# Performance work log

Measured on AMD Instinct MI355X. Metric: run time of the kernel, lower is better.

## Reference

```python
import jax, jax.numpy as jnp
import numpy as np

B, T, D, H = 4, 2048, 512, 8
K = D // H  # head dim = 64

def setup_inputs() -> dict:
    key = jax.random.key(0)
    k1, k2, k3, k4 = jax.random.split(key, 4)
    x = jax.random.normal(k1, (B, T, D), dtype=jnp.float32)
    # torch nn.Linear stores weight as [out_features, in_features]
    w_qkv = jax.random.normal(k2, (3 * D, D), dtype=jnp.float32) * (D ** -0.5)
    w_proj = jax.random.normal(k3, (D, D), dtype=jnp.float32) * (D ** -0.5)
    b_proj = jax.random.normal(k4, (D,), dtype=jnp.float32) * 0.01
    return {"x": x, "w_qkv": w_qkv, "w_proj": w_proj, "b_proj": b_proj}

def reference(x, w_qkv, w_proj, b_proj):
    Bx, Tx, Dx = x.shape
    # qkv projection (no bias): [B,T,3D]
    qkv = jnp.einsum('btd,ed->bte', x, w_qkv)
    q, k, v = jnp.split(qkv, 3, axis=-1)
    # [B,H,T,K]
    def heads(t):
        return t.reshape(Bx, Tx, H, K).transpose(0, 2, 1, 3)
    q, k, v = heads(q), heads(k), heads(v)
    # scaled scores with causal mask
    scores = jnp.einsum('bhqk,bhsk->bhqs', q, k) * (K ** -0.5)  # [B,H,T,T]
    causal = jnp.tril(jnp.ones((Tx, Tx), dtype=bool))
    scores = jnp.where(causal, scores, -jnp.inf)
    attn = jax.nn.softmax(scores, axis=-1)  # dropout p=0.0 -> identity
    out = jnp.einsum('bhqs,bhsk->bhqk', attn, v)  # [B,H,T,K]
    out = out.transpose(0, 2, 1, 3).reshape(Bx, Tx, Dx)
    out = jnp.einsum('btd,ed->bte', out, w_proj) + b_proj
    return out
```

## Files before the change

### kernel.cpp

```cpp
#include <hip/hip_runtime.h>
#include <hip/hip_bf16.h>


typedef unsigned short u16;
typedef __attribute__((ext_vector_type(8))) __bf16 bf16x8;
typedef __attribute__((ext_vector_type(8))) unsigned short u16x8;
typedef __attribute__((ext_vector_type(4))) unsigned short u16x4;
typedef __attribute__((ext_vector_type(4))) float f32x4;
typedef __attribute__((ext_vector_type(4))) unsigned u32x4;
typedef __attribute__((ext_vector_type(2))) unsigned u32x2;

#define DEV static __device__ __forceinline__

DEV void async16(const u16* g, u16* l) {
  __builtin_amdgcn_global_load_lds(
      (const __attribute__((address_space(1))) unsigned int*)g,
      (__attribute__((address_space(3))) unsigned int*)l, 16, 0, 0);
}
DEV u16x8 gld8(const u16* p) { return *(const u16x8*)p; }
DEV void lst8(u16* p, u16x8 v) { *(u16x8*)p = v; }
DEV bf16x8 ldsld8(const u16* p) {
  return __builtin_bit_cast(bf16x8, *(const u16x8*)p);
}
DEV f32x4 mfma16(bf16x8 a, bf16x8 b, f32x4 c) {
  return __builtin_amdgcn_mfma_f32_16x16x32_bf16(a, b, c, 0, 0, 0);
}
DEV u16 f2b(float f) {
  unsigned u = __builtin_bit_cast(unsigned, f);
  u += 0x7FFFu + ((u >> 16) & 1u);
  return (u16)(u >> 16);
}
DEV unsigned pk2(float x, float y) {
  __hip_bfloat162 t = __float22bfloat162_rn(float2{x, y});
  unsigned r;
  __builtin_memcpy(&r, &t, 4);
  return r;
}
DEV u16x8 pack8(f32x4 a, f32x4 b) {
  u32x4 t;
  t[0] = pk2(a[0], a[1]);
  t[1] = pk2(a[2], a[3]);
  t[2] = pk2(b[0], b[1]);
  t[3] = pk2(b[2], b[3]);
  return __builtin_bit_cast(u16x8, t);
}

__global__ void cvt_all(const float* __restrict__ x, const float* __restrict__ wq,
                        u16* __restrict__ xb, u16* __restrict__ wqb) {
  constexpr long NX = 8192L * 512 / 8;
  constexpr long NQ = 1536L * 512 / 8;
  const long i = (long)blockIdx.x * 256 + threadIdx.x;
  if (i < NX) {
    const float* p = x + i * 8;
    *(u16x8*)(xb + i * 8) = pack8(*(const f32x4*)p, *(const f32x4*)(p + 4));
  } else if (i < NX + NQ) {
    const long j = i - NX;
    const float* p = wq + j * 8;
    *(u16x8*)(wqb + j * 8) = pack8(*(const f32x4*)p, *(const f32x4*)(p + 4));
  }
}

__global__ void gemm_bb(const u16* __restrict__ A, const u16* __restrict__ Bt,
                        u16* __restrict__ qk, u16* __restrict__ vT, int K) {
  __shared__ __align__(16) u16 As[2][128 * 32];
  __shared__ __align__(16) u16 Bs[2][128 * 32];

  const int t = threadIdx.x, lane = t & 63, w = t >> 6;
  const int lane15 = lane & 15, quad = lane >> 4;
  const int wr = w >> 1, wc = w & 1;

  const int i = blockIdx.x;
  const int rt = (i & 7) | (((i >> 3) & 7) << 3);
  const int ct = i >> 6;
  const long row0 = (long)rt * 128;
  const int col0 = ct * 128;

  const int srow = w * 16 + (lane >> 2);
  const int scol = (lane & 3) * 8;
  const u16* Ag = A + (row0 + srow) * (long)K + scol;
  const u16* Bg = Bt + ((long)col0 + srow) * (long)K + scol;

  f32x4 acc[4][4];
#pragma unroll
  for (int ii = 0; ii < 4; ii++)
#pragma unroll
    for (int j = 0; j < 4; j++) acc[ii][j] = (f32x4)(0.0f);

  for (int k0 = 0; k0 < K; k0 += 64) {
    __syncthreads();
#pragma unroll
    for (int r = 0; r < 2; r++)
#pragma unroll
      for (int hf = 0; hf < 2; hf++) {
        async16(Ag + (long)r * 64 * K + k0 + hf * 32,
                &As[hf][(r * 64 + w * 16) * 32]);
        async16(Bg + (long)r * 64 * K + k0 + hf * 32,
                &Bs[hf][(r * 64 + w * 16) * 32]);
      }
    __syncthreads();

#pragma unroll
    for (int hf = 0; hf < 2; hf++) {
      bf16x8 a[4], b[4];
#pragma unroll
      for (int ii = 0; ii < 4; ii++)
        a[ii] = ldsld8(&As[hf][(wr * 64 + ii * 16 + lane15) * 32 + quad * 8]);
#pragma unroll
      for (int j = 0; j < 4; j++)
        b[j] = ldsld8(&Bs[hf][(wc * 64 + j * 16 + lane15) * 32 + quad * 8]);
#pragma unroll
      for (int ii = 0; ii < 4; ii++)
#pragma unroll
        for (int j = 0; j < 4; j++) acc[ii][j] = mfma16(a[ii], b[j], acc[ii][j]);
    }
  }

  if (col0 >= 1024) {
#pragma unroll
    for (int ii = 0; ii < 4; ii++)
#pragma unroll
      for (int j = 0; j < 4; j++) {
        const int hd = col0 - 1024 + wc * 64 + j * 16 + lane15;
        const long row = row0 + wr * 64 + ii * 16 + quad * 4;
        const long bb = row >> 11;
        const int s = (int)(row & 2047);
        u32x2 pr;
        pr[0] = pk2(acc[ii][j][0], acc[ii][j][1]);
        pr[1] = pk2(acc[ii][j][2], acc[ii][j][3]);
        *(u16x4*)(vT + (bb * 512 + hd) * 2048 + s) =
            __builtin_bit_cast(u16x4, pr);
      }
  } else {
#pragma unroll
    for (int ii = 0; ii < 4; ii++)
#pragma unroll
      for (int j = 0; j < 4; j++) {
        const int col = col0 + wc * 64 + j * 16 + lane15;
        const float sc = (col < 512) ? 0.18033688f : 1.0f;
#pragma unroll
        for (int r = 0; r < 4; r++) {
          const long row = row0 + wr * 64 + ii * 16 + quad * 4 + r;
          qk[row * 1024 + col] = f2b(acc[ii][j][r] * sc);
        }
      }
  }
}

__global__ void gemm_b64(const u16* __restrict__ A, const float* __restrict__ Bt,
                         const float* __restrict__ bias, float* __restrict__ C,
                         int N, int K) {
  __shared__ __align__(16) u16 As[2][128 * 32];
  __shared__ __align__(16) u16 Bs[2][64 * 32];

  const int t = threadIdx.x, lane = t & 63, w = t >> 6;
  const int lane15 = lane & 15, quad = lane >> 4;
  const int wr = w >> 1, wc = w & 1;

  const int i = blockIdx.x;
  const int rt = (i & 7) | (((i >> 3) & 7) << 3);
  const int ct = i >> 6;
  const long row0 = (long)rt * 128;
  const int col0 = ct * 64;

  const int srow = w * 16 + (lane >> 2);
  const int scol = (lane & 3) * 8;
  const u16* Ag = A + (row0 + srow) * (long)K + scol;

  const int brow = t >> 2, bc = (t & 3) * 16;
  const float* Bg = Bt + (long)(col0 + brow) * K + bc;
  u16* BsD = &Bs[bc >> 5][brow * 32 + (bc & 31)];

  f32x4 acc[4][2];
#pragma unroll
  for (int ii = 0; ii < 4; ii++)
#pragma unroll
    for (int j = 0; j < 2; j++) acc[ii][j] = (f32x4)(0.0f);

  f32x4 q0 = *(const f32x4*)Bg, q1 = *(const f32x4*)(Bg + 4);
  f32x4 q2 = *(const f32x4*)(Bg + 8), q3 = *(const f32x4*)(Bg + 12);

  for (int k0 = 0; k0 < K; k0 += 64) {
    __syncthreads();
#pragma unroll
    for (int r = 0; r < 2; r++)
#pragma unroll
      for (int hf = 0; hf < 2; hf++)
        async16(Ag + (long)r * 64 * K + k0 + hf * 32,
                &As[hf][(r * 64 + w * 16) * 32]);
    lst8(BsD, pack8(q0, q1));
    lst8(BsD + 8, pack8(q2, q3));
    __syncthreads();

    {
      const int kp = (k0 + 64 < K) ? k0 + 64 : k0;
      q0 = *(const f32x4*)(Bg + kp);     q1 = *(const f32x4*)(Bg + kp + 4);
      q2 = *(const f32x4*)(Bg + kp + 8); q3 = *(const f32x4*)(Bg + kp + 12);
    }

#pragma unroll
    for (int hf = 0; hf < 2; hf++) {
      bf16x8 a[4], b[2];
#pragma unroll
      for (int ii = 0; ii < 4; ii++)
        a[ii] = ldsld8(&As[hf][(wr * 64 + ii * 16 + lane15) * 32 + quad * 8]);
#pragma unroll
      for (int j = 0; j < 2; j++)
        b[j] = ldsld8(&Bs[hf][(wc * 32 + j * 16 + lane15) * 32 + quad * 8]);
#pragma unroll
      for (int ii = 0; ii < 4; ii++)
#pragma unroll
        for (int j = 0; j < 2; j++) acc[ii][j] = mfma16(a[ii], b[j], acc[ii][j]);
    }
  }

#pragma unroll
  for (int ii = 0; ii < 4; ii++)
#pragma unroll
    for (int j = 0; j < 2; j++) {
      const int col = col0 + wc * 32 + j * 16 + lane15;
      const float bv = bias[col];
#pragma unroll
      for (int r = 0; r < 4; r++) {
        const long row = row0 + wr * 64 + ii * 16 + quad * 4 + r;
        C[row * (long)N + col] = acc[ii][j][r] + bv;
      }
    }
}

__global__ void attn_v6(const u16* __restrict__ qk, const u16* __restrict__ vT,
                        u16* __restrict__ out) {
  constexpr int T = 2048, LDQ = 1024;
  __shared__ __align__(16) u16 Ks[64 * 72];
  __shared__ __align__(16) u16 Vs[64 * 72];
  __shared__ __align__(16) u16 Ps[4][16 * 72];

  const int t = threadIdx.x, lane = t & 63, w = t >> 6;
  const int lane15 = lane & 15, quad = lane >> 4;

  const int i = blockIdx.x;
  int qb = i & 31;
  if (i >= 512) qb = 31 - qb;
  const int h = (i >> 5) & 7;
  const int b = (i >> 8) & 3;
  const long baseq = (long)b * T * LDQ;
  const u16* vTb = vT + ((long)b * 512 + h * 64) * 2048;

  const u16* gq =
      qk + baseq + (long)(qb * 64 + w * 16 + lane15) * LDQ + h * 64 + quad * 8;
  const bf16x8 qa0 = __builtin_bit_cast(bf16x8, *(const u16x8*)gq);
  const bf16x8 qa1 = __builtin_bit_cast(bf16x8, *(const u16x8*)(gq + 32));

  const int srow = t >> 3, sc8 = (t & 7) * 8;

  const int nsb = qb + 1;

  u16x8 kr0, kr1, vr0, vr1;
  {
    const u16* gk = qk + baseq + (long)srow * LDQ + 512 + h * 64 + sc8;
    kr0 = gld8(gk); kr1 = gld8(gk + (long)32 * LDQ);
    const u16* gv = vTb + (long)srow * 2048 + sc8;
    vr0 = gld8(gv); vr1 = gld8(gv + (long)32 * 2048);
  }

  float lp[4] = {0.0f, 0.0f, 0.0f, 0.0f};
  f32x4 o[4];
#pragma unroll
  for (int j = 0; j < 4; j++) o[j] = (f32x4)(0.0f);

  const int qrow_base = qb * 64 + w * 16 + quad * 4;

  for (int sb = 0; sb < nsb; ++sb) {
    __syncthreads();
    lst8(&Ks[srow * 72 + sc8], kr0);
    lst8(&Ks[(srow + 32) * 72 + sc8], kr1);
    lst8(&Vs[srow * 72 + sc8], vr0);
    lst8(&Vs[(srow + 32) * 72 + sc8], vr1);
    __syncthreads();

    {
      const int sp = (sb + 1 < nsb) ? sb + 1 : sb;
      const u16* gk =
          qk + baseq + (long)(sp * 64 + srow) * LDQ + 512 + h * 64 + sc8;
      kr0 = gld8(gk); kr1 = gld8(gk + (long)32 * LDQ);
      const u16* gv = vTb + (long)srow * 2048 + sp * 64 + sc8;
      vr0 = gld8(gv); vr1 = gld8(gv + (long)32 * 2048);
    }

    f32x4 sf[4];
#pragma unroll
    for (int j = 0; j < 4; j++) {
      f32x4 z = (f32x4)(0.0f);
      z = mfma16(qa0, ldsld8(&Ks[(j * 16 + lane15) * 72 + quad * 8]), z);
      sf[j] = mfma16(qa1, ldsld8(&Ks[(j * 16 + lane15) * 72 + quad * 8 + 32]), z);
    }

    if (sb == qb) {
      const int scol_base = sb * 64 + lane15;
#pragma unroll
      for (int j = 0; j < 4; j++)
#pragma unroll
        for (int r = 0; r < 4; r++) {
          float p = exp2f(sf[j][r]);
          if (scol_base + j * 16 > qrow_base + r) p = 0.0f;
          sf[j][r] = p;
          lp[r] += p;
        }
    } else {
#pragma unroll
      for (int j = 0; j < 4; j++)
#pragma unroll
        for (int r = 0; r < 4; r++) {
          const float p = exp2f(sf[j][r]);
          sf[j][r] = p;
          lp[r] += p;
        }
    }

    u16* myP = Ps[w];
#pragma unroll
    for (int r = 0; r < 4; r++) {
      const int ro = (quad * 4 + r) * 72 + lane15;
      const unsigned v01 = pk2(sf[0][r], sf[1][r]);
      const unsigned v23 = pk2(sf[2][r], sf[3][r]);
      myP[ro] = (u16)v01;
      myP[ro + 16] = (u16)(v01 >> 16);
      myP[ro + 32] = (u16)v23;
      myP[ro + 48] = (u16)(v23 >> 16);
    }
    __asm__ __volatile__("" ::: "memory");
    const bf16x8 pa0 = ldsld8(&myP[lane15 * 72 + quad * 8]);
    const bf16x8 pa1 = ldsld8(&myP[lane15 * 72 + quad * 8 + 32]);
    __asm__ __volatile__("" ::: "memory");

#pragma unroll
    for (int j = 0; j < 4; j++) {
      const int d0 = (j * 16 + lane15) * 72;
      o[j] = mfma16(pa0, ldsld8(&Vs[d0 + quad * 8]), o[j]);
      o[j] = mfma16(pa1, ldsld8(&Vs[d0 + quad * 8 + 32]), o[j]);
    }
  }

#pragma unroll
  for (int off = 1; off < 16; off <<= 1)
#pragma unroll
    for (int r = 0; r < 4; r++) lp[r] += __shfl_xor(lp[r], off);

  const long orow0 = (long)b * T + qb * 64 + w * 16;
  float inv[4];
#pragma unroll
  for (int r = 0; r < 4; r++) inv[r] = 1.0f / lp[r];
#pragma unroll
  for (int j = 0; j < 4; j++)
#pragma unroll
    for (int r = 0; r < 4; r++)
      out[(orow0 + quad * 4 + r) * 512 + h * 64 + j * 16 + lane15] =
          f2b(o[j][r] * inv[r]);
}

extern "C" void kernel_launch(void* const* d_in, const int* in_sizes, int n_in,
                              void* d_out, int out_size, void* d_ws, size_t ws_size,
                              hipStream_t stream) {
  const float* x      = (const float*)d_in[0];
  const float* w_qkv  = (const float*)d_in[1];
  const float* w_proj = (const float*)d_in[2];
  const float* b_proj = (const float*)d_in[3];
  float* out = (float*)d_out;

  u16* qk = (u16*)d_ws;
  u16* vT = qk + (size_t)8192 * 1024;
  u16* xb = vT + (size_t)4 * 512 * 2048;
  u16* wqb = (u16*)d_out;

  cvt_all<<<2432, 256, 0, stream>>>(x, w_qkv, xb, wqb);
  gemm_bb<<<768, 256, 0, stream>>>(xb, wqb, qk, vT, 512);
  attn_v6<<<1024, 256, 0, stream>>>(qk, vT, xb);
  gemm_b64<<<512, 256, 0, stream>>>(xb, w_proj, b_proj, out, 512, 512);
}
```

Measured before the change: 153.9 us.

## Fuse fp32-to-bf16 conversion into QKV GEMM and shrink output GEMM tiles

Removes the separate conversion kernel: the QKV GEMM now reads fp32 x and w_qkv directly, converts them to bf16 in registers, and register-prefetches the next K tile before storing it to LDS, replacing the async global-to-LDS copies. This drops one launch and the write and re-read of the bf16 copies, but adds the conversion work to every tile load, and the weight is now re-converted by every block that reads it. Separately, the output projection GEMM moves from 128x64 to 64x64 tiles with twice as many blocks, to raise occupancy for the 512-wide output.

```diff
diff --git a/kernel.cpp b/kernel.cpp
--- a/kernel.cpp
+++ b/kernel.cpp
@@ -45,23 +45,8 @@
   return __builtin_bit_cast(u16x8, t);
 }
 
-__global__ void cvt_all(const float* __restrict__ x, const float* __restrict__ wq,
-                        u16* __restrict__ xb, u16* __restrict__ wqb) {
-  constexpr long NX = 8192L * 512 / 8;
-  constexpr long NQ = 1536L * 512 / 8;
-  const long i = (long)blockIdx.x * 256 + threadIdx.x;
-  if (i < NX) {
-    const float* p = x + i * 8;
-    *(u16x8*)(xb + i * 8) = pack8(*(const f32x4*)p, *(const f32x4*)(p + 4));
-  } else if (i < NX + NQ) {
-    const long j = i - NX;
-    const float* p = wq + j * 8;
-    *(u16x8*)(wqb + j * 8) = pack8(*(const f32x4*)p, *(const f32x4*)(p + 4));
-  }
-}
-
-__global__ void gemm_bb(const u16* __restrict__ A, const u16* __restrict__ Bt,
-                        u16* __restrict__ qk, u16* __restrict__ vT, int K) {
+__global__ void gemm1f(const float* __restrict__ A, const float* __restrict__ Bt,
+                       u16* __restrict__ qk, u16* __restrict__ vT, int K) {
   __shared__ __align__(16) u16 As[2][128 * 32];
   __shared__ __align__(16) u16 Bs[2][128 * 32];
 
@@ -75,10 +60,18 @@
   const long row0 = (long)rt * 128;
   const int col0 = ct * 128;
 
-  const int srow = w * 16 + (lane >> 2);
-  const int scol = (lane & 3) * 8;
-  const u16* Ag = A + (row0 + srow) * (long)K + scol;
-  const u16* Bg = Bt + ((long)col0 + srow) * (long)K + scol;
+  const int sr = t >> 2, sc = (t & 3) * 8;
+  const float* Ag = A + (row0 + sr) * (long)K + sc;
+  const float* Bg = Bt + (long)(col0 + sr) * K + sc;
+  u16* AsD[2][2];
+  u16* BsD[2][2];
+#pragma unroll
+  for (int r = 0; r < 2; r++)
+#pragma unroll
+    for (int hf = 0; hf < 2; hf++) {
+      AsD[r][hf] = &As[hf][(sr + r * 64) * 32 + sc];
+      BsD[r][hf] = &Bs[hf][(sr + r * 64) * 32 + sc];
+    }
 
   f32x4 acc[4][4];
 #pragma unroll
@@ -86,18 +79,40 @@
 #pragma unroll
     for (int j = 0; j < 4; j++) acc[ii][j] = (f32x4)(0.0f);
 
+  u16x8 ra[2][2], rb[2][2];
+#pragma unroll
+  for (int r = 0; r < 2; r++)
+#pragma unroll
+    for (int hf = 0; hf < 2; hf++) {
+      const float* pa = Ag + (long)r * 64 * K + hf * 32;
+      const float* pb = Bg + (long)r * 64 * K + hf * 32;
+      ra[r][hf] = pack8(*(const f32x4*)pa, *(const f32x4*)(pa + 4));
+      rb[r][hf] = pack8(*(const f32x4*)pb, *(const f32x4*)(pb + 4));
+    }
+
   for (int k0 = 0; k0 < K; k0 += 64) {
     __syncthreads();
 #pragma unroll
     for (int r = 0; r < 2; r++)
 #pragma unroll
       for (int hf = 0; hf < 2; hf++) {
-        async16(Ag + (long)r * 64 * K + k0 + hf * 32,
-                &As[hf][(r * 64 + w * 16) * 32]);
-        async16(Bg + (long)r * 64 * K + k0 + hf * 32,
-                &Bs[hf][(r * 64 + w * 16) * 32]);
+        lst8(AsD[r][hf], ra[r][hf]);
+        lst8(BsD[r][hf], rb[r][hf]);
       }
     __syncthreads();
+
+    {
+      const int kp = (k0 + 64 < K) ? k0 + 64 : k0;
+#pragma unroll
+      for (int r = 0; r < 2; r++)
+#pragma unroll
+        for (int hf = 0; hf < 2; hf++) {
+          const float* pa = Ag + (long)r * 64 * K + kp + hf * 32;
+          const float* pb = Bg + (long)r * 64 * K + kp + hf * 32;
+          ra[r][hf] = pack8(*(const f32x4*)pa, *(const f32x4*)(pa + 4));
+          rb[r][hf] = pack8(*(const f32x4*)pb, *(const f32x4*)(pb + 4));
+        }
+    }
 
 #pragma unroll
     for (int hf = 0; hf < 2; hf++) {
@@ -136,20 +151,20 @@
 #pragma unroll
       for (int j = 0; j < 4; j++) {
         const int col = col0 + wc * 64 + j * 16 + lane15;
-        const float sc = (col < 512) ? 0.18033688f : 1.0f;
+        const float sc2 = (col < 512) ? 0.18033688f : 1.0f;
 #pragma unroll
         for (int r = 0; r < 4; r++) {
           const long row = row0 + wr * 64 + ii * 16 + quad * 4 + r;
-          qk[row * 1024 + col] = f2b(acc[ii][j][r] * sc);
+          qk[row * 1024 + col] = f2b(acc[ii][j][r] * sc2);
         }
       }
   }
 }
 
-__global__ void gemm_b64(const u16* __restrict__ A, const float* __restrict__ Bt,
+__global__ void gemm3_64(const u16* __restrict__ A, const float* __restrict__ Bt,
                          const float* __restrict__ bias, float* __restrict__ C,
                          int N, int K) {
-  __shared__ __align__(16) u16 As[2][128 * 32];
+  __shared__ __align__(16) u16 As[2][64 * 32];
   __shared__ __align__(16) u16 Bs[2][64 * 32];
 
   const int t = threadIdx.x, lane = t & 63, w = t >> 6;
@@ -157,22 +172,20 @@
   const int wr = w >> 1, wc = w & 1;
 
   const int i = blockIdx.x;
-  const int rt = (i & 7) | (((i >> 3) & 7) << 3);
-  const int ct = i >> 6;
-  const long row0 = (long)rt * 128;
+  const int rt = (i & 7) | (((i >> 3) & 15) << 3);
+  const int ct = i >> 7;
+  const long row0 = (long)rt * 64;
   const int col0 = ct * 64;
 
-  const int srow = w * 16 + (lane >> 2);
-  const int scol = (lane & 3) * 8;
-  const u16* Ag = A + (row0 + srow) * (long)K + scol;
+  const u16* Ag = A + (row0 + w * 16 + (lane >> 2)) * (long)K + (lane & 3) * 8;
 
   const int brow = t >> 2, bc = (t & 3) * 16;
   const float* Bg = Bt + (long)(col0 + brow) * K + bc;
   u16* BsD = &Bs[bc >> 5][brow * 32 + (bc & 31)];
 
-  f32x4 acc[4][2];
-#pragma unroll
-  for (int ii = 0; ii < 4; ii++)
+  f32x4 acc[2][2];
+#pragma unroll
+  for (int ii = 0; ii < 2; ii++)
 #pragma unroll
     for (int j = 0; j < 2; j++) acc[ii][j] = (f32x4)(0.0f);
 
@@ -182,11 +195,8 @@
   for (int k0 = 0; k0 < K; k0 += 64) {
     __syncthreads();
 #pragma unroll
-    for (int r = 0; r < 2; r++)
-#pragma unroll
-      for (int hf = 0; hf < 2; hf++)
-        async16(Ag + (long)r * 64 * K + k0 + hf * 32,
-                &As[hf][(r * 64 + w * 16) * 32]);
+    for (int hf = 0; hf < 2; hf++)
+      async16(Ag + k0 + hf * 32, &As[hf][(w * 16) * 32]);
     lst8(BsD, pack8(q0, q1));
     lst8(BsD + 8, pack8(q2, q3));
     __syncthreads();
@@ -199,29 +209,29 @@
 
 #pragma unroll
     for (int hf = 0; hf < 2; hf++) {
-      bf16x8 a[4], b[2];
-#pragma unroll
-      for (int ii = 0; ii < 4; ii++)
-        a[ii] = ldsld8(&As[hf][(wr * 64 + ii * 16 + lane15) * 32 + quad * 8]);
+      bf16x8 a[2], b[2];
+#pragma unroll
+      for (int ii = 0; ii < 2; ii++)
+        a[ii] = ldsld8(&As[hf][(wr * 32 + ii * 16 + lane15) * 32 + quad * 8]);
 #pragma unroll
       for (int j = 0; j < 2; j++)
         b[j] = ldsld8(&Bs[hf][(wc * 32 + j * 16 + lane15) * 32 + quad * 8]);
 #pragma unroll
-      for (int ii = 0; ii < 4; ii++)
+      for (int ii = 0; ii < 2; ii++)
 #pragma unroll
         for (int j = 0; j < 2; j++) acc[ii][j] = mfma16(a[ii], b[j], acc[ii][j]);
     }
   }
 
 #pragma unroll
-  for (int ii = 0; ii < 4; ii++)
+  for (int ii = 0; ii < 2; ii++)
 #pragma unroll
     for (int j = 0; j < 2; j++) {
       const int col = col0 + wc * 32 + j * 16 + lane15;
       const float bv = bias[col];
 #pragma unroll
       for (int r = 0; r < 4; r++) {
-        const long row = row0 + wr * 64 + ii * 16 + quad * 4 + r;
+        const long row = row0 + wr * 32 + ii * 16 + quad * 4 + r;
         C[row * (long)N + col] = acc[ii][j][r] + bv;
       }
     }
@@ -369,10 +379,8 @@
   u16* qk = (u16*)d_ws;
   u16* vT = qk + (size_t)8192 * 1024;
   u16* xb = vT + (size_t)4 * 512 * 2048;
-  u16* wqb = (u16*)d_out;
-
-  cvt_all<<<2432, 256, 0, stream>>>(x, w_qkv, xb, wqb);
-  gemm_bb<<<768, 256, 0, stream>>>(xb, wqb, qk, vT, 512);
+
+  gemm1f<<<768, 256, 0, stream>>>(x, w_qkv, qk, vT, 512);
   attn_v6<<<1024, 256, 0, stream>>>(qk, vT, xb);
-  gemm_b64<<<512, 256, 0, stream>>>(xb, w_proj, b_proj, out, 512, 512);
-}
+  gemm3_64<<<1024, 256, 0, stream>>>(xb, w_proj, b_proj, out, 512, 512);
+}
```

Measured after the change: 218.1 us. 41.7% more time.
